# Optimization experiments

Hardware: AMD Instinct MI355X
Metric: run time of the kernel (lower is better)

The kernel has to match this reference:

```python
import jax, jax.numpy as jnp
import numpy as np

EMBED = 1024
HEADS = 16
HEAD_DIM = EMBED // HEADS
MLP_DIM = 4096
EPS = 1e-5


def setup_inputs() -> dict:
    key = jax.random.key(0)
    ks = jax.random.split(key, 12)
    s = lambda d: 1.0 / np.sqrt(d)
    return {
        "x": jax.random.normal(ks[0], (8, 1024, EMBED), dtype=jnp.float32),
        "ln1_g": jnp.ones((EMBED,), jnp.float32),
        "ln1_b": jnp.zeros((EMBED,), jnp.float32),
        "w_qkv": jax.random.normal(ks[1], (EMBED, 3 * EMBED), jnp.float32) * s(EMBED),
        "b_qkv": jnp.zeros((3 * EMBED,), jnp.float32),
        "w_proj": jax.random.normal(ks[2], (EMBED, EMBED), jnp.float32) * s(EMBED),
        "b_proj": jnp.zeros((EMBED,), jnp.float32),
        "ln2_g": jnp.ones((EMBED,), jnp.float32),
        "ln2_b": jnp.zeros((EMBED,), jnp.float32),
        "w_fc1": jax.random.normal(ks[3], (EMBED, MLP_DIM), jnp.float32) * s(EMBED),
        "b_fc1": jnp.zeros((MLP_DIM,), jnp.float32),
        "w_fc2": jax.random.normal(ks[4], (MLP_DIM, EMBED), jnp.float32) * s(MLP_DIM),
        "b_fc2": jnp.zeros((EMBED,), jnp.float32),
    }


def _layernorm(x, g, b):
    mu = jnp.mean(x, axis=-1, keepdims=True)
    var = jnp.mean(jnp.square(x - mu), axis=-1, keepdims=True)
    return (x - mu) * jax.lax.rsqrt(var + EPS) * g + b


def reference(x, ln1_g, ln1_b, w_qkv, b_qkv, w_proj, b_proj,
              ln2_g, ln2_b, w_fc1, b_fc1, w_fc2, b_fc2):
    B, N, D = x.shape
    scale = HEAD_DIM ** -0.5

    # --- attention branch ---
    h = _layernorm(x, ln1_g, ln1_b)
    qkv = h @ w_qkv + b_qkv                       # [B,N,3D]
    qkv = qkv.reshape(B, N, 3, HEADS, HEAD_DIM)
    q, k, v = jnp.moveaxis(qkv, 2, 0)             # each [B,N,H,hd]
    attn = jnp.einsum('bqhd,bkhd->bhqk', q, k) * scale
    attn = jax.nn.softmax(attn, axis=-1)
    out = jnp.einsum('bhqk,bkhd->bqhd', attn, v).reshape(B, N, D)
    x = x + (out @ w_proj + b_proj)

    # --- MLP branch ---
    h = _layernorm(x, ln2_g, ln2_b)
    h = jax.nn.gelu(h @ w_fc1 + b_fc1, approximate=False)
    x = x + (h @ w_fc2 + b_fc2)
    return x
```

## Files before the change

### kernel.cpp

```cpp
#include <hip/hip_runtime.h>
#include <cstdint>


typedef unsigned short u16;
typedef short short8 __attribute__((ext_vector_type(8)));
typedef float floatx4 __attribute__((ext_vector_type(4)));

#define GLB(p) ((const __attribute__((address_space(1))) void*)(p))
#define LDSP(p) ((__attribute__((address_space(3))) void*)(p))

__device__ __forceinline__ u16 f2bf(float f) {
    uint32_t u = __float_as_uint(f);
    u += 0x7fffu + ((u >> 16) & 1u);
    return (u16)(u >> 16);
}
__device__ __forceinline__ uint32_t pack2(float a, float b) {
    return (uint32_t)f2bf(a) | ((uint32_t)f2bf(b) << 16);
}
__device__ __forceinline__ float fast_gelu(float v) {
    float u = v * (0.7978845608f + 0.0356774081f * v * v);
    float e = __expf(2.0f * u);
    float th = 1.0f - 2.0f * __builtin_amdgcn_rcpf(e + 1.0f);
    return 0.5f * v * (1.0f + th);
}

__global__ __launch_bounds__(256) void transpose_cast_kernel(
    const float* __restrict__ W, u16* __restrict__ Wt, int K, int N)
{
    __shared__ float tile[32][33];
    int n0 = blockIdx.x * 32, k0 = blockIdx.y * 32;
    int tx = threadIdx.x, ty = threadIdx.y;
    #pragma unroll
    for (int i = 0; i < 4; ++i)
        tile[ty + i * 8][tx] = W[(size_t)(k0 + ty + i * 8) * N + n0 + tx];
    __syncthreads();
    #pragma unroll
    for (int i = 0; i < 4; ++i)
        Wt[(size_t)(n0 + ty + i * 8) * K + k0 + tx] = f2bf(tile[tx][ty + i * 8]);
}

__global__ __launch_bounds__(256) void ln_kernel(
    const float* __restrict__ x, const float* __restrict__ gw,
    const float* __restrict__ bw, u16* __restrict__ out)
{
    const int row = blockIdx.x, tid = threadIdx.x;
    float4 v = ((const float4*)(x + (size_t)row * 1024))[tid];
    float s  = v.x + v.y + v.z + v.w;
    float ss = v.x * v.x + v.y * v.y + v.z * v.z + v.w * v.w;
    #pragma unroll
    for (int off = 32; off > 0; off >>= 1) {
        s  += __shfl_down(s, off);
        ss += __shfl_down(ss, off);
    }
    __shared__ float red[8];
    if ((tid & 63) == 0) { red[tid >> 6] = s; red[4 + (tid >> 6)] = ss; }
    __syncthreads();
    float S  = red[0] + red[1] + red[2] + red[3];
    float SS = red[4] + red[5] + red[6] + red[7];
    float mu  = S * (1.0f / 1024.0f);
    float var = SS * (1.0f / 1024.0f) - mu * mu;
    float rs  = rsqrtf(var + 1e-5f);
    float4 g4 = ((const float4*)gw)[tid];
    float4 b4 = ((const float4*)bw)[tid];
    u16* o = out + (size_t)row * 1024 + tid * 4;
    o[0] = f2bf((v.x - mu) * rs * g4.x + b4.x);
    o[1] = f2bf((v.y - mu) * rs * g4.y + b4.y);
    o[2] = f2bf((v.z - mu) * rs * g4.z + b4.z);
    o[3] = f2bf((v.w - mu) * rs * g4.w + b4.w);
}

#define MODE_BF16      0
#define MODE_BF16_GELU 1
#define MODE_F32_RES   2
#define MODE_QKV       3

#define G3_BUFSZ 24576
#define G3_LDS_BYTES 147456

template<int MODE>
__global__ __launch_bounds__(512, 2) void gemm3_kernel(
    const u16* __restrict__ A, const u16* __restrict__ Bt,
    const float* __restrict__ bias, const float* __restrict__ res,
    void* __restrict__ outv, u16* __restrict__ vt, int M, int N, int K)
{
    extern __shared__ u16 lds[];
    const int tid = threadIdx.x;
    const int wave = tid >> 6, lane = tid & 63;
    const int lg = lane >> 4, lc = lane & 15;
    const int m0 = blockIdx.y * 256, n0 = blockIdx.x * 128;
    const int wr = wave >> 1, wc = wave & 1;

    floatx4 acc[4][4];
    #pragma unroll
    for (int i = 0; i < 4; ++i)
        #pragma unroll
        for (int j = 0; j < 4; ++j) acc[i][j] = floatx4{0.f, 0.f, 0.f, 0.f};

    const int srow = lane >> 3;
    const int schunk = (lane & 7) ^ srow;

    const u16* gsrc[6];
    int ldsoff[6];
    #pragma unroll
    for (int j = 0; j < 6; ++j) {
        const int g = wave * 6 + j;
        if (g < 32) {
            gsrc[j]   = A  + (size_t)(m0 + g * 8 + srow) * K + schunk * 8;
            ldsoff[j] = g * 512;
        } else {
            gsrc[j]   = Bt + (size_t)(n0 + (g - 32) * 8 + srow) * K + schunk * 8;
            ldsoff[j] = 16384 + (g - 32) * 512;
        }
    }

    const int nt = K >> 6;
    auto stage = [&](int b, int kk) {
        u16* base = lds + b * G3_BUFSZ;
        #pragma unroll
        for (int j = 0; j < 6; ++j)
            __builtin_amdgcn_global_load_lds(GLB(gsrc[j] + kk), LDSP(base + ldsoff[j]), 16, 0, 0);
    };

    stage(0, 0);
    stage(1, 64);
    asm volatile("s_waitcnt vmcnt(6)" ::: "memory");
    __builtin_amdgcn_s_barrier();
    __builtin_amdgcn_sched_barrier(0);

    int cur = 0;
    for (int t = 0; t < nt; ++t) {
        const int tn = t + 2;
        const int kk = (tn < nt ? tn : nt - 1) << 6;
        const int nb = (cur >= 1) ? cur - 1 : cur + 2;
        stage(nb, kk);

        const u16* Ab = lds + cur * G3_BUFSZ;
        const u16* Bb = Ab + 16384;
        #pragma unroll
        for (int ks = 0; ks < 2; ++ks) {
            short8 fa[4], fb[4];
            #pragma unroll
            for (int mt = 0; mt < 4; ++mt)
                fa[mt] = *(const short8*)&Ab[(wr * 64 + mt * 16 + lc) * 64 +
                                             (((ks * 4 + lg) ^ (lc & 7)) * 8)];
            #pragma unroll
            for (int nn = 0; nn < 4; ++nn)
                fb[nn] = *(const short8*)&Bb[(wc * 64 + nn * 16 + lc) * 64 +
                                             (((ks * 4 + lg) ^ (lc & 7)) * 8)];
            __builtin_amdgcn_s_setprio(1);
            #pragma unroll
            for (int mt = 0; mt < 4; ++mt)
                #pragma unroll
                for (int nn = 0; nn < 4; ++nn)
                    acc[mt][nn] = __builtin_amdgcn_mfma_f32_16x16x32_bf16(fa[mt], fb[nn], acc[mt][nn], 0, 0, 0);
            __builtin_amdgcn_s_setprio(0);
        }
        asm volatile("s_waitcnt vmcnt(6)" ::: "memory");
        __builtin_amdgcn_s_barrier();
        __builtin_amdgcn_sched_barrier(0);
        cur = (cur + 1 == 3) ? 0 : cur + 1;
    }

    if (MODE == MODE_QKV && n0 >= 2048) {
        #pragma unroll
        for (int mt = 0; mt < 4; ++mt) {
            #pragma unroll
            for (int nn = 0; nn < 4; ++nn) {
                const int col = n0 + wc * 64 + nn * 16 + lc;
                const float bv = bias[col];
                const int hd = col - 2048;
                const int rowbase = m0 + wr * 64 + mt * 16 + lg * 4;
                const int b = rowbase >> 10, token = rowbase & 1023;
                float v0 = acc[mt][nn][0] + bv, v1 = acc[mt][nn][1] + bv;
                float v2 = acc[mt][nn][2] + bv, v3 = acc[mt][nn][3] + bv;
                uint2 pk = {pack2(v0, v1), pack2(v2, v3)};
                *(uint2*)&vt[((size_t)b * 1024 + hd) * 1024 + token] = pk;
            }
        }
        return;
    }
    #pragma unroll
    for (int mt = 0; mt < 4; ++mt) {
        #pragma unroll
        for (int nn = 0; nn < 4; ++nn) {
            const int col = n0 + wc * 64 + nn * 16 + lc;
            const float bv = bias[col];
            #pragma unroll
            for (int r = 0; r < 4; ++r) {
                const int row = m0 + wr * 64 + mt * 16 + lg * 4 + r;
                float v = acc[mt][nn][r] + bv;
                if (MODE == MODE_BF16 || MODE == MODE_QKV) {
                    ((u16*)outv)[(size_t)row * N + col] = f2bf(v);
                } else if (MODE == MODE_BF16_GELU) {
                    ((u16*)outv)[(size_t)row * N + col] = f2bf(fast_gelu(v));
                } else {
                    ((float*)outv)[(size_t)row * N + col] = v + res[(size_t)row * N + col];
                }
            }
        }
    }
}

__global__ __launch_bounds__(256) void attn_kernel(
    const u16* __restrict__ qkv, const u16* __restrict__ vtg, u16* __restrict__ out)
{
    const int bid = blockIdx.x;
    const int g = ((bid >> 7) << 3) | (bid & 7);
    const int qt = (bid >> 3) & 15;
    const int h = g & 15, b = g >> 4;
    const int tid = threadIdx.x, wave = tid >> 6, lane = tid & 63;
    const int lg = lane >> 4, lc = lane & 15;

    __shared__ __attribute__((aligned(16))) u16 Qs[64 * 64];
    __shared__ __attribute__((aligned(16))) u16 Ks[64 * 64];
    __shared__ __attribute__((aligned(16))) u16 Vts[64 * 64];
    __shared__ __attribute__((aligned(16))) u16 Ps[64 * 64];

    const int q0 = qt * 64;
    const size_t hb = ((size_t)b * 1024) * 3072 + h * 64;
    const u16* vhead = vtg + ((size_t)b * 1024 + h * 64) * 1024;
    const int srow = lane >> 3;
    const int schunk = (lane & 7) ^ srow;

    {
        const u16* Qg = qkv + hb + (size_t)(q0 + wave * 16 + srow) * 3072 + schunk * 8;
        u16* Qw = &Qs[wave * 1024];
        __builtin_amdgcn_global_load_lds(GLB(Qg), LDSP(Qw), 16, 0, 0);
        __builtin_amdgcn_global_load_lds(GLB(Qg + (size_t)8 * 3072), LDSP(Qw + 512), 16, 0, 0);
    }
    __syncthreads();
    short8 aq[2];
    aq[0] = *(const short8*)&Qs[(wave * 16 + lc) * 64 + (((0 + lg) ^ (lc & 7)) * 8)];
    aq[1] = *(const short8*)&Qs[(wave * 16 + lc) * 64 + (((4 + lg) ^ (lc & 7)) * 8)];

    floatx4 o[4];
    #pragma unroll
    for (int dt = 0; dt < 4; ++dt) o[dt] = floatx4{0.f, 0.f, 0.f, 0.f};
    float mprev = -INFINITY, lsum = 0.f;
    const float sc = 0.125f;

    for (int kt = 0; kt < 16; ++kt) {
        __syncthreads();
        {
            const u16* Kg = qkv + hb + 1024 +
                (size_t)(kt * 64 + wave * 16 + srow) * 3072 + schunk * 8;
            u16* Kw = &Ks[wave * 1024];
            __builtin_amdgcn_global_load_lds(GLB(Kg), LDSP(Kw), 16, 0, 0);
            __builtin_amdgcn_global_load_lds(GLB(Kg + (size_t)8 * 3072), LDSP(Kw + 512), 16, 0, 0);
        }
        {
            const u16* Vg = vhead + (size_t)(wave * 16 + srow) * 1024 + kt * 64 + schunk * 8;
            u16* Vw = &Vts[wave * 1024];
            __builtin_amdgcn_global_load_lds(GLB(Vg), LDSP(Vw), 16, 0, 0);
            __builtin_amdgcn_global_load_lds(GLB(Vg + (size_t)8 * 1024), LDSP(Vw + 512), 16, 0, 0);
        }
        __syncthreads();

        floatx4 st[4];
        #pragma unroll
        for (int nt = 0; nt < 4; ++nt) st[nt] = floatx4{0.f, 0.f, 0.f, 0.f};
        #pragma unroll
        for (int ks = 0; ks < 2; ++ks)
            #pragma unroll
            for (int nt = 0; nt < 4; ++nt) {
                short8 fk = *(const short8*)&Ks[(nt * 16 + lc) * 64 +
                                                (((ks * 4 + lg) ^ (lc & 7)) * 8)];
                st[nt] = __builtin_amdgcn_mfma_f32_16x16x32_bf16(fk, aq[ks], st[nt], 0, 0, 0);
            }

        float m = st[0][0];
        #pragma unroll
        for (int nt = 0; nt < 4; ++nt)
            #pragma unroll
            for (int r = 0; r < 4; ++r) m = fmaxf(m, st[nt][r]);
        m = fmaxf(m, __shfl_xor(m, 16));
        m = fmaxf(m, __shfl_xor(m, 32));
        float mn = fmaxf(mprev, m * sc);
        float aexp = __expf(mprev - mn);
        mprev = mn;

        const int q = wave * 16 + lc;
        float rs = 0.f;
        #pragma unroll
        for (int nt = 0; nt < 4; ++nt) {
            float p0 = __expf(st[nt][0] * sc - mn);
            float p1 = __expf(st[nt][1] * sc - mn);
            float p2 = __expf(st[nt][2] * sc - mn);
            float p3 = __expf(st[nt][3] * sc - mn);
            rs += (p0 + p1) + (p2 + p3);
            const int c16 = nt * 2 + (lg >> 1);
            uint2 pk = {pack2(p0, p1), pack2(p2, p3)};
            *(uint2*)&Ps[q * 64 + ((c16 ^ (lc & 7)) * 8) + (lg & 1) * 4] = pk;
        }
        rs += __shfl_xor(rs, 16);
        rs += __shfl_xor(rs, 32);
        lsum = lsum * aexp + rs;
        #pragma unroll
        for (int dt = 0; dt < 4; ++dt)
            #pragma unroll
            for (int r = 0; r < 4; ++r) o[dt][r] *= aexp;

        #pragma unroll
        for (int ks = 0; ks < 2; ++ks) {
            short8 fp = *(const short8*)&Ps[q * 64 + (((ks * 4 + lg) ^ (lc & 7)) * 8)];
            #pragma unroll
            for (int dt = 0; dt < 4; ++dt) {
                short8 fv = *(const short8*)&Vts[(dt * 16 + lc) * 64 +
                                                 (((ks * 4 + lg) ^ (lc & 7)) * 8)];
                o[dt] = __builtin_amdgcn_mfma_f32_16x16x32_bf16(fv, fp, o[dt], 0, 0, 0);
            }
        }
    }

    const float rl = 1.0f / lsum;
    const int q = q0 + wave * 16 + lc;
    #pragma unroll
    for (int dt = 0; dt < 4; ++dt) {
        uint2 pk = {pack2(o[dt][0] * rl, o[dt][1] * rl),
                    pack2(o[dt][2] * rl, o[dt][3] * rl)};
        *(uint2*)&out[((size_t)b * 1024 + q) * 1024 + h * 64 + dt * 16 + lg * 4] = pk;
    }
}

extern "C" void kernel_launch(void* const* d_in, const int* in_sizes, int n_in,
                              void* d_out, int out_size, void* d_ws, size_t ws_size,
                              hipStream_t stream)
{
    const float* x      = (const float*)d_in[0];
    const float* ln1_g  = (const float*)d_in[1];
    const float* ln1_b  = (const float*)d_in[2];
    const float* w_qkv  = (const float*)d_in[3];
    const float* b_qkv  = (const float*)d_in[4];
    const float* w_proj = (const float*)d_in[5];
    const float* b_proj = (const float*)d_in[6];
    const float* ln2_g  = (const float*)d_in[7];
    const float* ln2_b  = (const float*)d_in[8];
    const float* w_fc1  = (const float*)d_in[9];
    const float* b_fc1  = (const float*)d_in[10];
    const float* w_fc2  = (const float*)d_in[11];
    const float* b_fc2  = (const float*)d_in[12];
    float* outp = (float*)d_out;

    char* ws = (char*)d_ws;
    size_t off = 0;
    auto alloc = [&](size_t bytes) { void* p = ws + off; off += (bytes + 255) & ~(size_t)255; return p; };
    u16*  wqkvT  = (u16*)alloc((size_t)3072 * 1024 * 2);
    u16*  wprojT = (u16*)alloc((size_t)1024 * 1024 * 2);
    u16*  wfc1T  = (u16*)alloc((size_t)4096 * 1024 * 2);
    u16*  wfc2T  = (u16*)alloc((size_t)1024 * 4096 * 2);
    u16*  hbuf   = (u16*)alloc((size_t)8192 * 1024 * 2);
    u16*  big    = (u16*)alloc((size_t)8192 * 4096 * 2);
    u16*  vtbuf  = (u16*)alloc((size_t)8 * 1024 * 1024 * 2);
    u16*  attno  = (u16*)alloc((size_t)8192 * 1024 * 2);
    float* x2    = (float*)alloc((size_t)8192 * 1024 * 4);

    static bool attr_done = []{
        hipFuncSetAttribute(reinterpret_cast<const void*>(gemm3_kernel<MODE_QKV>),
                            hipFuncAttributeMaxDynamicSharedMemorySize, G3_LDS_BYTES);
        hipFuncSetAttribute(reinterpret_cast<const void*>(gemm3_kernel<MODE_BF16_GELU>),
                            hipFuncAttributeMaxDynamicSharedMemorySize, G3_LDS_BYTES);
        hipFuncSetAttribute(reinterpret_cast<const void*>(gemm3_kernel<MODE_F32_RES>),
                            hipFuncAttributeMaxDynamicSharedMemorySize, G3_LDS_BYTES);
        return true;
    }();
    (void)attr_done;

    dim3 tb(32, 8);
    transpose_cast_kernel<<<dim3(3072 / 32, 1024 / 32), tb, 0, stream>>>(w_qkv,  wqkvT,  1024, 3072);
    transpose_cast_kernel<<<dim3(1024 / 32, 1024 / 32), tb, 0, stream>>>(w_proj, wprojT, 1024, 1024);
    transpose_cast_kernel<<<dim3(4096 / 32, 1024 / 32), tb, 0, stream>>>(w_fc1,  wfc1T,  1024, 4096);
    transpose_cast_kernel<<<dim3(1024 / 32, 4096 / 32), tb, 0, stream>>>(w_fc2,  wfc2T,  4096, 1024);

    ln_kernel<<<8192, 256, 0, stream>>>(x, ln1_g, ln1_b, hbuf);
    gemm3_kernel<MODE_QKV><<<dim3(3072 / 128, 8192 / 256), 512, G3_LDS_BYTES, stream>>>(
        hbuf, wqkvT, b_qkv, nullptr, big, vtbuf, 8192, 3072, 1024);
    attn_kernel<<<2048, 256, 0, stream>>>(big, vtbuf, attno);
    gemm3_kernel<MODE_F32_RES><<<dim3(1024 / 128, 8192 / 256), 512, G3_LDS_BYTES, stream>>>(
        attno, wprojT, b_proj, x, x2, nullptr, 8192, 1024, 1024);
    ln_kernel<<<8192, 256, 0, stream>>>(x2, ln2_g, ln2_b, hbuf);
    gemm3_kernel<MODE_BF16_GELU><<<dim3(4096 / 128, 8192 / 256), 512, G3_LDS_BYTES, stream>>>(
        hbuf, wfc1T, b_fc1, nullptr, big, nullptr, 8192, 4096, 1024);
    gemm3_kernel<MODE_F32_RES><<<dim3(1024 / 128, 8192 / 256), 512, G3_LDS_BYTES, stream>>>(
        big, wfc2T, b_fc2, x2, outp, nullptr, 8192, 1024, 4096);
}
```

Measured before the change: 513.4 us.

## Enlarge GEMM tiles to 256x256, switch to double buffering, split fc2 over K

Each GEMM block now computes a 256x256 output tile with 8x4 accumulator fragments per wave instead of 256x128, which raises operand reuse per LDS load. The triple-buffered LDS pipeline becomes a double-buffered one: the next stage is issued only after a barrier following compute, and waits use lgkmcnt/vmcnt. The fc2 GEMM is split into two sequential K-halves through a new F32_ACC mode, with the partial sum kept in the reused vt/attention-output workspace. The risk is that proj and fc2 now launch only 128 blocks on a 256-CU GPU, only one 128KB-LDS block fits per CU, and the K-split adds an extra fp32 round trip without adding parallelism.

```diff
diff --git a/kernel.cpp b/kernel.cpp
--- a/kernel.cpp
+++ b/kernel.cpp
@@ -73,103 +73,107 @@
 #define MODE_BF16_GELU 1
 #define MODE_F32_RES   2
 #define MODE_QKV       3
-
-#define G3_BUFSZ 24576
-#define G3_LDS_BYTES 147456
+#define MODE_F32_ACC   4
+
+#define G3_BUFSZ 32768
+#define G3_LDS_BYTES 131072
 
 template<int MODE>
 __global__ __launch_bounds__(512, 2) void gemm3_kernel(
     const u16* __restrict__ A, const u16* __restrict__ Bt,
     const float* __restrict__ bias, const float* __restrict__ res,
-    void* __restrict__ outv, u16* __restrict__ vt, int M, int N, int K)
+    void* __restrict__ outv, u16* __restrict__ vt,
+    int M, int N, int lda, int ldb, int K)
 {
     extern __shared__ u16 lds[];
     const int tid = threadIdx.x;
     const int wave = tid >> 6, lane = tid & 63;
     const int lg = lane >> 4, lc = lane & 15;
-    const int m0 = blockIdx.y * 256, n0 = blockIdx.x * 128;
-    const int wr = wave >> 1, wc = wave & 1;
-
-    floatx4 acc[4][4];
-    #pragma unroll
-    for (int i = 0; i < 4; ++i)
+    const int m0 = blockIdx.y * 256, n0 = blockIdx.x * 256;
+    const int wr = wave >> 2, wc = wave & 3;
+
+    floatx4 acc[8][4];
+    #pragma unroll
+    for (int i = 0; i < 8; ++i)
         #pragma unroll
         for (int j = 0; j < 4; ++j) acc[i][j] = floatx4{0.f, 0.f, 0.f, 0.f};
 
     const int srow = lane >> 3;
     const int schunk = (lane & 7) ^ srow;
 
-    const u16* gsrc[6];
-    int ldsoff[6];
-    #pragma unroll
-    for (int j = 0; j < 6; ++j) {
-        const int g = wave * 6 + j;
-        if (g < 32) {
-            gsrc[j]   = A  + (size_t)(m0 + g * 8 + srow) * K + schunk * 8;
-            ldsoff[j] = g * 512;
-        } else {
-            gsrc[j]   = Bt + (size_t)(n0 + (g - 32) * 8 + srow) * K + schunk * 8;
-            ldsoff[j] = 16384 + (g - 32) * 512;
-        }
-    }
+    const u16* Agl = A  + (size_t)(m0 + wave * 32 + srow) * lda + schunk * 8;
+    const u16* Bgl = Bt + (size_t)(n0 + wave * 32 + srow) * ldb + schunk * 8;
+    const size_t a8 = (size_t)8 * lda, b8 = (size_t)8 * ldb;
 
     const int nt = K >> 6;
     auto stage = [&](int b, int kk) {
         u16* base = lds + b * G3_BUFSZ;
         #pragma unroll
-        for (int j = 0; j < 6; ++j)
-            __builtin_amdgcn_global_load_lds(GLB(gsrc[j] + kk), LDSP(base + ldsoff[j]), 16, 0, 0);
+        for (int j = 0; j < 4; ++j)
+            __builtin_amdgcn_global_load_lds(GLB(Agl + kk + j * a8),
+                                             LDSP(base + (wave * 4 + j) * 512), 16, 0, 0);
+        #pragma unroll
+        for (int j = 0; j < 4; ++j)
+            __builtin_amdgcn_global_load_lds(GLB(Bgl + kk + j * b8),
+                                             LDSP(base + 16384 + (wave * 4 + j) * 512), 16, 0, 0);
     };
 
     stage(0, 0);
     stage(1, 64);
-    asm volatile("s_waitcnt vmcnt(6)" ::: "memory");
+    asm volatile("s_waitcnt vmcnt(8)" ::: "memory");
     __builtin_amdgcn_s_barrier();
     __builtin_amdgcn_sched_barrier(0);
 
     int cur = 0;
     for (int t = 0; t < nt; ++t) {
-        const int tn = t + 2;
-        const int kk = (tn < nt ? tn : nt - 1) << 6;
-        const int nb = (cur >= 1) ? cur - 1 : cur + 2;
-        stage(nb, kk);
-
         const u16* Ab = lds + cur * G3_BUFSZ;
         const u16* Bb = Ab + 16384;
         #pragma unroll
         for (int ks = 0; ks < 2; ++ks) {
-            short8 fa[4], fb[4];
-            #pragma unroll
-            for (int mt = 0; mt < 4; ++mt)
-                fa[mt] = *(const short8*)&Ab[(wr * 64 + mt * 16 + lc) * 64 +
-                                             (((ks * 4 + lg) ^ (lc & 7)) * 8)];
+            short8 fb[4];
             #pragma unroll
             for (int nn = 0; nn < 4; ++nn)
                 fb[nn] = *(const short8*)&Bb[(wc * 64 + nn * 16 + lc) * 64 +
                                              (((ks * 4 + lg) ^ (lc & 7)) * 8)];
-            __builtin_amdgcn_s_setprio(1);
-            #pragma unroll
-            for (int mt = 0; mt < 4; ++mt)
+            #pragma unroll
+            for (int mh = 0; mh < 2; ++mh) {
+                short8 fa[4];
                 #pragma unroll
-                for (int nn = 0; nn < 4; ++nn)
-                    acc[mt][nn] = __builtin_amdgcn_mfma_f32_16x16x32_bf16(fa[mt], fb[nn], acc[mt][nn], 0, 0, 0);
-            __builtin_amdgcn_s_setprio(0);
-        }
-        asm volatile("s_waitcnt vmcnt(6)" ::: "memory");
+                for (int mt = 0; mt < 4; ++mt)
+                    fa[mt] = *(const short8*)&Ab[(wr * 128 + mh * 64 + mt * 16 + lc) * 64 +
+                                                 (((ks * 4 + lg) ^ (lc & 7)) * 8)];
+                __builtin_amdgcn_s_setprio(1);
+                #pragma unroll
+                for (int mt = 0; mt < 4; ++mt)
+                    #pragma unroll
+                    for (int nn = 0; nn < 4; ++nn)
+                        acc[mh * 4 + mt][nn] = __builtin_amdgcn_mfma_f32_16x16x32_bf16(
+                            fa[mt], fb[nn], acc[mh * 4 + mt][nn], 0, 0, 0);
+                __builtin_amdgcn_s_setprio(0);
+            }
+        }
+        asm volatile("s_waitcnt lgkmcnt(0)" ::: "memory");
         __builtin_amdgcn_s_barrier();
         __builtin_amdgcn_sched_barrier(0);
-        cur = (cur + 1 == 3) ? 0 : cur + 1;
+        {
+            const int tn = (t + 2 < nt) ? t + 2 : nt - 1;
+            stage(cur, tn << 6);
+        }
+        asm volatile("s_waitcnt vmcnt(8)" ::: "memory");
+        __builtin_amdgcn_s_barrier();
+        __builtin_amdgcn_sched_barrier(0);
+        cur ^= 1;
     }
 
     if (MODE == MODE_QKV && n0 >= 2048) {
         #pragma unroll
-        for (int mt = 0; mt < 4; ++mt) {
+        for (int mt = 0; mt < 8; ++mt) {
             #pragma unroll
             for (int nn = 0; nn < 4; ++nn) {
                 const int col = n0 + wc * 64 + nn * 16 + lc;
                 const float bv = bias[col];
                 const int hd = col - 2048;
-                const int rowbase = m0 + wr * 64 + mt * 16 + lg * 4;
+                const int rowbase = m0 + wr * 128 + mt * 16 + lg * 4;
                 const int b = rowbase >> 10, token = rowbase & 1023;
                 float v0 = acc[mt][nn][0] + bv, v1 = acc[mt][nn][1] + bv;
                 float v2 = acc[mt][nn][2] + bv, v3 = acc[mt][nn][3] + bv;
@@ -180,14 +184,14 @@
         return;
     }
     #pragma unroll
-    for (int mt = 0; mt < 4; ++mt) {
+    for (int mt = 0; mt < 8; ++mt) {
         #pragma unroll
         for (int nn = 0; nn < 4; ++nn) {
             const int col = n0 + wc * 64 + nn * 16 + lc;
-            const float bv = bias[col];
+            const float bv = (MODE == MODE_F32_ACC) ? 0.f : bias[col];
             #pragma unroll
             for (int r = 0; r < 4; ++r) {
-                const int row = m0 + wr * 64 + mt * 16 + lg * 4 + r;
+                const int row = m0 + wr * 128 + mt * 16 + lg * 4 + r;
                 float v = acc[mt][nn][r] + bv;
                 if (MODE == MODE_BF16 || MODE == MODE_QKV) {
                     ((u16*)outv)[(size_t)row * N + col] = f2bf(v);
@@ -353,6 +357,7 @@
     u16*  vtbuf  = (u16*)alloc((size_t)8 * 1024 * 1024 * 2);
     u16*  attno  = (u16*)alloc((size_t)8192 * 1024 * 2);
     float* x2    = (float*)alloc((size_t)8192 * 1024 * 4);
+    float* pbuf  = (float*)vtbuf;
 
     static bool attr_done = []{
         hipFuncSetAttribute(reinterpret_cast<const void*>(gemm3_kernel<MODE_QKV>),
@@ -361,6 +366,8 @@
                             hipFuncAttributeMaxDynamicSharedMemorySize, G3_LDS_BYTES);
         hipFuncSetAttribute(reinterpret_cast<const void*>(gemm3_kernel<MODE_F32_RES>),
                             hipFuncAttributeMaxDynamicSharedMemorySize, G3_LDS_BYTES);
+        hipFuncSetAttribute(reinterpret_cast<const void*>(gemm3_kernel<MODE_F32_ACC>),
+                            hipFuncAttributeMaxDynamicSharedMemorySize, G3_LDS_BYTES);
         return true;
     }();
     (void)attr_done;
@@ -372,14 +379,16 @@
     transpose_cast_kernel<<<dim3(1024 / 32, 4096 / 32), tb, 0, stream>>>(w_fc2,  wfc2T,  4096, 1024);
 
     ln_kernel<<<8192, 256, 0, stream>>>(x, ln1_g, ln1_b, hbuf);
-    gemm3_kernel<MODE_QKV><<<dim3(3072 / 128, 8192 / 256), 512, G3_LDS_BYTES, stream>>>(
-        hbuf, wqkvT, b_qkv, nullptr, big, vtbuf, 8192, 3072, 1024);
+    gemm3_kernel<MODE_QKV><<<dim3(3072 / 256, 8192 / 256), 512, G3_LDS_BYTES, stream>>>(
+        hbuf, wqkvT, b_qkv, nullptr, big, vtbuf, 8192, 3072, 1024, 1024, 1024);
     attn_kernel<<<2048, 256, 0, stream>>>(big, vtbuf, attno);
-    gemm3_kernel<MODE_F32_RES><<<dim3(1024 / 128, 8192 / 256), 512, G3_LDS_BYTES, stream>>>(
-        attno, wprojT, b_proj, x, x2, nullptr, 8192, 1024, 1024);
+    gemm3_kernel<MODE_F32_RES><<<dim3(1024 / 256, 8192 / 256), 512, G3_LDS_BYTES, stream>>>(
+        attno, wprojT, b_proj, x, x2, nullptr, 8192, 1024, 1024, 1024, 1024);
     ln_kernel<<<8192, 256, 0, stream>>>(x2, ln2_g, ln2_b, hbuf);
-    gemm3_kernel<MODE_BF16_GELU><<<dim3(4096 / 128, 8192 / 256), 512, G3_LDS_BYTES, stream>>>(
-        hbuf, wfc1T, b_fc1, nullptr, big, nullptr, 8192, 4096, 1024);
-    gemm3_kernel<MODE_F32_RES><<<dim3(1024 / 128, 8192 / 256), 512, G3_LDS_BYTES, stream>>>(
-        big, wfc2T, b_fc2, x2, outp, nullptr, 8192, 1024, 4096);
-}
+    gemm3_kernel<MODE_BF16_GELU><<<dim3(4096 / 256, 8192 / 256), 512, G3_LDS_BYTES, stream>>>(
+        hbuf, wfc1T, b_fc1, nullptr, big, nullptr, 8192, 4096, 1024, 1024, 1024);
+    gemm3_kernel<MODE_F32_RES><<<dim3(1024 / 256, 8192 / 256), 512, G3_LDS_BYTES, stream>>>(
+        big, wfc2T, b_fc2, x2, pbuf, nullptr, 8192, 1024, 4096, 4096, 2048);
+    gemm3_kernel<MODE_F32_ACC><<<dim3(1024 / 256, 8192 / 256), 512, G3_LDS_BYTES, stream>>>(
+        big + 2048, wfc2T + 2048, nullptr, pbuf, outp, nullptr, 8192, 1024, 4096, 4096, 2048);
+}
```

New measurement: 554.1 us. 1.08x slower.
